# Performance work log

Measured on AMD Instinct MI355X. Metric: run time of the kernel, lower is better.

The kernel has to match this reference:

```python
import jax, jax.numpy as jnp
import numpy as np

B, N, D, H, A = 1024, 8, 256, 512, 4  # batch, num_objects, embedding_dim, hidden_dim, action_dim


def _edge_list(batch, n):
    # Fully connected (no self-loops) over n nodes, replicated per sample with offset b*n.
    pairs = np.array([(i, j) for i in range(n) for j in range(n) if i != j], dtype=np.int32)
    off = (np.arange(batch, dtype=np.int32) * n)[:, None]
    row = (pairs[:, 0][None, :] + off).reshape(-1)
    col = (pairs[:, 1][None, :] + off).reshape(-1)
    return jnp.asarray(row), jnp.asarray(col)


def _layer_norm(x, g, b):
    m = x.mean(-1, keepdims=True)
    v = x.var(-1, keepdims=True)
    return (x - m) / jnp.sqrt(v + 1e-5) * g + b


def _mlp(x, w1, b1, w2, b2, g, bn, w3, b3):
    h = jax.nn.relu(x @ w1 + b1)
    h = jax.nn.relu(_layer_norm(h @ w2 + b2, g, bn))
    return h @ w3 + b3


def setup_inputs() -> dict:
    key = jax.random.key(0)
    ks = jax.random.split(key, 12)
    def w(k, shape):
        return jax.random.normal(k, shape, jnp.float32) / np.sqrt(shape[0]).astype(np.float32)
    return {
        "states": jax.random.normal(ks[0], (B, N, D), jnp.float32),
        "action": jax.random.randint(ks[1], (B,), 0, A),
        # edge MLP: 3D -> H -> H (LN) -> H
        "e_w1": w(ks[2], (3 * D, H)), "e_b1": jnp.zeros((H,), jnp.float32),
        "e_w2": w(ks[3], (H, H)),     "e_b2": jnp.zeros((H,), jnp.float32),
        "e_g":  jnp.ones((H,), jnp.float32), "e_bn": jnp.zeros((H,), jnp.float32),
        "e_w3": w(ks[4], (H, H)),     "e_b3": jnp.zeros((H,), jnp.float32),
        # node MLP: H + D + A -> H -> H (LN) -> D
        "n_w1": w(ks[5], (H + D + A, H)), "n_b1": jnp.zeros((H,), jnp.float32),
        "n_w2": w(ks[6], (H, H)),         "n_b2": jnp.zeros((H,), jnp.float32),
        "n_g":  jnp.ones((H,), jnp.float32), "n_bn": jnp.zeros((H,), jnp.float32),
        "n_w3": w(ks[7], (H, D)),         "n_b3": jnp.zeros((D,), jnp.float32),
    }


def reference(states, action,
              e_w1, e_b1, e_w2, e_b2, e_g, e_bn, e_w3, e_b3,
              n_w1, n_b1, n_w2, n_b2, n_g, n_bn, n_w3, n_b3):
    eP = (e_w1, e_b1, e_w2, e_b2, e_g, e_bn, e_w3, e_b3)
    nP = (n_w1, n_b1, n_w2, n_b2, n_g, n_bn, n_w3, n_b3)
    flat = states.reshape(-1, D)                       # [B*N, D]
    row, col = _edge_list(B, N - 1)                    # faithful: edge list over N-1 objects
    E = row.shape[0]
    # copy_action / embodied: one-hot action repeated per object
    av = jnp.repeat(jax.nn.one_hot(action, A, dtype=flat.dtype), N, axis=0)  # [B*N, A]
    # round 0: edge_attr starts as zeros like node features
    e = _mlp(jnp.concatenate([flat[row], jnp.zeros((E, D), flat.dtype), flat[col]], 1), *eP)
    agg = jax.ops.segment_sum(e, row, num_segments=B * N)  # [B*N, H]
    node = _mlp(jnp.concatenate([flat, av, agg], 1), *nP)   # [B*N, D]
    flat = flat + node
    av0 = jnp.zeros_like(av)
    for _ in range(N - 1):
        e = _mlp(jnp.concatenate([flat[row], node[row], flat[col]], 1), *eP)
        agg = jax.ops.segment_sum(e, row, num_segments=B * N)
        node = _mlp(jnp.concatenate([flat, av0, agg], 1), *nP)
        flat = flat + node
    return flat.reshape(B, N, D)
```

## Files before the change

### kernel.cpp

```cpp
#include <hip/hip_runtime.h>
#include <cstddef>

typedef _Float16 f16x8 __attribute__((ext_vector_type(8)));
typedef _Float16 f16x4 __attribute__((ext_vector_type(4)));
typedef float f32x16 __attribute__((ext_vector_type(16)));
typedef unsigned short ushort_t;

#define NSEG 7168
#define NNODE 8192

enum { EP_NONE = 0, EP_BIAS = 1, EP_RAWP = 2, EP_NL1 = 3, EP_NL3 = 4 };

#define PHASE_BARRIER() do { asm volatile("s_waitcnt lgkmcnt(0)" ::: "memory"); \
                             __builtin_amdgcn_s_barrier(); } while (0)

#define RELU8(v) do { _Pragma("unroll") \
  for (int j_ = 0; j_ < 8; ++j_) v[j_] = v[j_] > (_Float16)0 ? v[j_] : (_Float16)0; } while (0)

__global__ __launch_bounds__(256)
void prepack(const float* __restrict__ W, ushort_t* __restrict__ P,
             int koff, int kcnt, int Nsrc, int NTpack, int noff) {
  int idx = blockIdx.x * 256 + threadIdx.x;
  if (idx >= kcnt * Nsrc) return;
  int kl = idx / Nsrc, n = idx - kl * Nsrc + noff;
  _Float16 h = (_Float16)W[idx];
  int k = koff + kl;
  size_t o = ((((size_t)(k >> 4)) * NTpack + (n >> 5)) * 64 + ((k >> 3) & 1) * 32 + (n & 31)) * 8 + (k & 7);
  P[o] = __builtin_bit_cast(ushort_t, h);
}

__global__ __launch_bounds__(256)
void v6k(const float* __restrict__ eb3, const float* __restrict__ nw1,
         float* __restrict__ v6) {
  int n = blockIdx.x * 256 + threadIdx.x;
  if (n >= 512) return;
  float a = 0.f;
  for (int k = 0; k < 512; ++k) a += eb3[k] * nw1[(size_t)(260 + k) * 512 + n];
  v6[n] = 6.f * a;
}

template <int NCOLB, int EPI, int EDGE, int LNIN, int X1F16, int OUTF16>
__global__ __launch_bounds__(256, 4)
void gemmT(const void* __restrict__ X1v, int ld1, int nph1,
           const void* __restrict__ X2v, int ld2, int nph2,
           const ushort_t* __restrict__ Sm, const ushort_t* __restrict__ Tm,
           const ushort_t* __restrict__ P,
           const float* __restrict__ bias, const float* __restrict__ bias2,
           const int* __restrict__ action, const float* __restrict__ wact,
           const float* __restrict__ lnpart,
           const float* __restrict__ lng, const float* __restrict__ lnbn,
           void* __restrict__ Yv, float* __restrict__ Yres,
           float* __restrict__ Part, int m0base) {
  constexpr int N = NCOLB * 128;
  constexpr int NT = N / 32;
  const int u = threadIdx.x;
  const int nwg = gridDim.x;
  const int qq = nwg >> 3, r8 = nwg & 7;
  const int xcd = blockIdx.x & 7, inx = blockIdx.x >> 3;
  const int logical = (xcd < r8 ? xcd * (qq + 1) : r8 * (qq + 1) + (xcd - r8) * qq) + inx;
  const int mY = (logical / NCOLB) * 64;
  const int cb = logical - (logical / NCOLB) * NCOLB;
  const int nB = cb * 128;
  const int lane = u & 63, w = u >> 6;
  const int wr = w >> 1, wc = w & 1;
  const int r31 = lane & 31, rt2 = lane >> 5;

  __shared__ ushort_t lA[16384];

  const int kcA = w * 2, kcB = w * 2 + 1;
  const int widx0 = (((rt2 * 8 + kcA) * 2 + 0) * 32 + (r31 ^ ((kcA & 3) << 3))) * 8;
  const int widx1 = (((rt2 * 8 + kcA) * 2 + 1) * 32 + (r31 ^ ((kcA & 3) << 3))) * 8;
  const int widx2 = (((rt2 * 8 + kcB) * 2 + 0) * 32 + (r31 ^ ((kcB & 3) << 3))) * 8;
  const int widx3 = (((rt2 * 8 + kcB) * 2 + 1) * 32 + (r31 ^ ((kcB & 3) << 3))) * 8;

  const ushort_t* sB = nullptr;
  const ushort_t* tB = nullptr;
  const float* x1f = nullptr;
  const ushort_t* x1h = nullptr;
  const ushort_t* x2h = nullptr;
  if (EDGE) {
    int e = m0base + mY + lane;
    int b = e / 42, p = e - b * 42;
    int i = p / 6, tt = p - i * 6;
    int j = tt + (tt >= i ? 1 : 0);
    sB = Sm + (size_t)(b * 7 + i) * 1024 + w * 32;
    tB = Tm + (size_t)(b * 7 + j) * 1024 + w * 32;
  } else {
    if (X1F16) x1h = (const ushort_t*)X1v + (size_t)(mY + lane) * ld1 + w * 32;
    else       x1f = (const float*)X1v + (size_t)(mY + lane) * ld1 + w * 32;
    if (nph2 > 0) x2h = (const ushort_t*)X2v + (size_t)(mY + lane) * ld2 + w * 32;
  }
  float mym = 0.f, myr = 0.f;
  if (LNIN) {
    const float* pp = lnpart + (size_t)(mY + lane) * 16;
    float S_ = 0.f, Q_ = 0.f;
    #pragma unroll
    for (int i = 0; i < 8; ++i) { S_ += pp[i]; Q_ += pp[8 + i]; }
    mym = S_ * (1.f / 512.f);
    myr = rsqrtf(Q_ * (1.f / 512.f) - mym * mym + 1e-5f);
  }

  f16x8 xc0, xc1, xc2, xc3;
  auto loadx = [&](int ph) {
    if (EDGE) {
      const ushort_t* sp = sB + ph * 128;
      const ushort_t* tp = tB + ph * 128;
      f16x8 s0 = *(const f16x8*)sp,        t0 = *(const f16x8*)tp;
      f16x8 s1 = *(const f16x8*)(sp + 8),  t1 = *(const f16x8*)(tp + 8);
      f16x8 s2 = *(const f16x8*)(sp + 16), t2 = *(const f16x8*)(tp + 16);
      f16x8 s3 = *(const f16x8*)(sp + 24), t3 = *(const f16x8*)(tp + 24);
      xc0 = s0 + t0; xc1 = s1 + t1; xc2 = s2 + t2; xc3 = s3 + t3;
      RELU8(xc0); RELU8(xc1); RELU8(xc2); RELU8(xc3);
    } else if (!X1F16 && ph < nph1) {
      const float* src = x1f + ph * 128;
      float4 l0 = *(const float4*)(src +  0), h0 = *(const float4*)(src +  4);
      float4 l1 = *(const float4*)(src +  8), h1 = *(const float4*)(src + 12);
      float4 l2 = *(const float4*)(src + 16), h2 = *(const float4*)(src + 20);
      float4 l3 = *(const float4*)(src + 24), h3 = *(const float4*)(src + 28);
#define CVT8(X, lo, hi) do { X[0]=(_Float16)lo.x; X[1]=(_Float16)lo.y; \
      X[2]=(_Float16)lo.z; X[3]=(_Float16)lo.w; X[4]=(_Float16)hi.x; \
      X[5]=(_Float16)hi.y; X[6]=(_Float16)hi.z; X[7]=(_Float16)hi.w; } while (0)
      CVT8(xc0, l0, h0); CVT8(xc1, l1, h1); CVT8(xc2, l2, h2); CVT8(xc3, l3, h3);
#undef CVT8
    } else {
      const ushort_t* src = (ph < nph1) ? x1h + ph * 128 : x2h + (ph - nph1) * 128;
      xc0 = *(const f16x8*)src;
      xc1 = *(const f16x8*)(src + 8);
      xc2 = *(const f16x8*)(src + 16);
      xc3 = *(const f16x8*)(src + 24);
      if (LNIN) {
        const int kb = ph * 128 + w * 32;
#define LN8(X, OFS) do { _Pragma("unroll") for (int j_ = 0; j_ < 8; ++j_) { \
        float xx = (float)X[j_]; \
        xx = fmaxf((xx - mym) * myr * lng[kb + (OFS) + j_] + lnbn[kb + (OFS) + j_], 0.f); \
        X[j_] = (_Float16)xx; } } while (0)
        LN8(xc0, 0); LN8(xc1, 8); LN8(xc2, 16); LN8(xc3, 24);
#undef LN8
      }
    }
  };
  auto cvtwrite = [&](int b) {
    const int base = b * 8192;
    *(f16x8*)&lA[base + widx0] = xc0;
    *(f16x8*)&lA[base + widx1] = xc1;
    *(f16x8*)&lA[base + widx2] = xc2;
    *(f16x8*)&lA[base + widx3] = xc3;
  };

  f32x16 acc0, acc1;
  #pragma unroll
  for (int q = 0; q < 16; ++q) { acc0[q] = 0.f; acc1[q] = 0.f; }

  const int nph = nph1 + nph2;
  const int ntb = (nB >> 5) + wc * 2;
  const int TOT = nph * 8;

#define LOADA(S, A_) do { \
    const int aofs_ = lbase + (((wr * 8 + (S)) * 2 + rt2) * 32 + (r31 ^ (((S) & 3) << 3))) * 8; \
    A_ = *(const f16x8*)&lA[aofs_]; } while (0)

#define LOADB(G_, H0, H1) do { \
    const ushort_t* bp_ = P + (((size_t)(G_) * NT + ntb) * 64 + lane) * 8; \
    H0 = *(const f16x8*)bp_; \
    H1 = *(const f16x8*)(bp_ + 512); } while (0)

#define MFMA2(AH, H0, H1) do { \
    acc0 = __builtin_amdgcn_mfma_f32_32x32x16_f16(AH, H0, acc0, 0, 0, 0); \
    acc1 = __builtin_amdgcn_mfma_f32_32x32x16_f16(AH, H1, acc1, 0, 0, 0); } while (0)

  loadx(0);
  cvtwrite(0);
  if (nph > 1) loadx(1);
  PHASE_BARRIER();
  f16x8 b00, b01, b10, b11, b20, b21, b30, b31;
  LOADB(0, b00, b01);
  LOADB(1, b10, b11);
  LOADB(2, b20, b21);
  LOADB(3, b30, b31);

  #pragma unroll 1
  for (int ph = 0; ph < nph; ++ph) {
    if (ph + 1 < nph) {
      cvtwrite((ph + 1) & 1);
      if (ph + 2 < nph) loadx(ph + 2);
    }
    const int lbase = (ph & 1) * 8192;
    const int g0 = ph * 8;
    f16x8 ac, an;
    LOADA(0, ac);
#define STEP(S, BH, BL) do { \
    if ((S) < 7) LOADA((S) + 1, an); \
    f16x8 h0 = BH, h1 = BL; \
    if (g0 + (S) + 4 < TOT) LOADB(g0 + (S) + 4, BH, BL); \
    MFMA2(ac, h0, h1); \
    if ((S) < 7) ac = an; } while (0)
    STEP(0, b00, b01);
    STEP(1, b10, b11);
    STEP(2, b20, b21);
    STEP(3, b30, b31);
    STEP(4, b00, b01);
    STEP(5, b10, b11);
    STEP(6, b20, b21);
    STEP(7, b30, b31);
#undef STEP
    if (ph + 1 < nph) PHASE_BARRIER();
  }

  const int col0 = nB + wc * 64 + r31;
  float v[2][16];
  {
    float bc0 = (EPI == EP_NONE) ? 0.f : bias[col0];
    float bc1 = (EPI == EP_NONE) ? 0.f : bias[col0 + 32];
    #pragma unroll
    for (int q = 0; q < 16; ++q) {
      v[0][q] = acc0[q] + bc0;
      v[1][q] = acc1[q] + bc1;
    }
  }

  if (EPI == EP_NL1) {
    #pragma unroll
    for (int q = 0; q < 16; ++q) {
      int m = mY + wr * 32 + (q & 3) + 8 * (q >> 2) + 4 * rt2;
      if (m < NSEG) {
        v[0][q] += bias2[col0];
        v[1][q] += bias2[col0 + 32];
      }
      if (action != nullptr) {
        const float* wrp = wact + (size_t)(256 + action[m >> 3]) * 512;
        v[0][q] += wrp[col0];
        v[1][q] += wrp[col0 + 32];
      }
    }
    #pragma unroll
    for (int ct = 0; ct < 2; ++ct)
      #pragma unroll
      for (int q = 0; q < 16; ++q) v[ct][q] = fmaxf(v[ct][q], 0.f);
  }

  if (EPI == EP_RAWP) {
    float sv[16], qv[16];
    #pragma unroll
    for (int q = 0; q < 16; ++q) {
      sv[q] = v[0][q] + v[1][q];
      qv[q] = v[0][q] * v[0][q] + v[1][q] * v[1][q];
    }
    #pragma unroll
    for (int mm = 1; mm <= 16; mm <<= 1) {
      #pragma unroll
      for (int q = 0; q < 16; ++q) {
        sv[q] += __shfl_xor(sv[q], mm);
        qv[q] += __shfl_xor(qv[q], mm);
      }
    }
    if (r31 == 0) {
      #pragma unroll
      for (int q = 0; q < 16; ++q) {
        int m = mY + wr * 32 + (q & 3) + 8 * (q >> 2) + 4 * rt2;
        Part[(size_t)m * 16 + cb * 2 + wc] = sv[q];
        Part[(size_t)m * 16 + 8 + cb * 2 + wc] = qv[q];
      }
    }
  }

  #pragma unroll
  for (int ct = 0; ct < 2; ++ct) {
    #pragma unroll
    for (int q = 0; q < 16; ++q) {
      int m = mY + wr * 32 + (q & 3) + 8 * (q >> 2) + 4 * rt2;
      float z = v[ct][q];
      if (OUTF16)
        ((ushort_t*)Yv)[(size_t)m * N + col0 + ct * 32] =
            __builtin_bit_cast(ushort_t, (_Float16)z);
      else
        ((float*)Yv)[(size_t)m * N + col0 + ct * 32] = z;
      if (EPI == EP_NL3) Yres[(size_t)m * N + col0 + ct * 32] += z;
    }
  }
#undef LOADA
#undef LOADB
#undef MFMA2
}

__global__ __launch_bounds__(256)
void h2_sum_ln(const ushort_t* __restrict__ H2, const float* __restrict__ Part,
               const float* __restrict__ g, const float* __restrict__ bn,
               ushort_t* __restrict__ SS) {
  __shared__ float smu[12], srs[12];
  const int u = threadIdx.x;
  const int g2 = blockIdx.x * 2;
  if (u < 12) {
    const float* pp = Part + ((size_t)g2 * 6 + u) * 16;
    float S = 0.f, Q = 0.f;
    #pragma unroll
    for (int i = 0; i < 8; ++i) { S += pp[i]; Q += pp[8 + i]; }
    float m = S * (1.f / 512.f);
    smu[u] = m;
    srs[u] = rsqrtf(Q * (1.f / 512.f) - m * m + 1e-5f);
  }
  __syncthreads();
  const int ln = g2 + (u >> 7);
  const int lloc = (u >> 7) * 6;
  const int c4 = (u & 127) * 4;
  float4 gv = *(const float4*)(g + c4);
  float4 bv = *(const float4*)(bn + c4);
  float a0 = 0.f, a1 = 0.f, a2 = 0.f, a3 = 0.f;
  #pragma unroll
  for (int r = 0; r < 6; ++r) {
    int row = ln * 6 + r;
    f16x4 y = *(const f16x4*)(H2 + (size_t)row * 512 + c4);
    float m = smu[lloc + r], rs = srs[lloc + r];
    a0 += fmaxf(((float)y[0] - m) * rs * gv.x + bv.x, 0.f);
    a1 += fmaxf(((float)y[1] - m) * rs * gv.y + bv.y, 0.f);
    a2 += fmaxf(((float)y[2] - m) * rs * gv.z + bv.z, 0.f);
    a3 += fmaxf(((float)y[3] - m) * rs * gv.w + bv.w, 0.f);
  }
  f16x4 o;
  o[0] = (_Float16)a0; o[1] = (_Float16)a1; o[2] = (_Float16)a2; o[3] = (_Float16)a3;
  *(f16x4*)(SS + (size_t)ln * 512 + c4) = o;
}

extern "C" void kernel_launch(void* const* d_in, const int* in_sizes, int n_in,
                              void* d_out, int out_size, void* d_ws, size_t ws_size,
                              hipStream_t stream) {
  (void)in_sizes; (void)n_in; (void)out_size;
  const float* states = (const float*)d_in[0];
  const int* action = (const int*)d_in[1];
  const float* e_w1 = (const float*)d_in[2];
  const float* e_b1 = (const float*)d_in[3];
  const float* e_w2 = (const float*)d_in[4];
  const float* e_b2 = (const float*)d_in[5];
  const float* e_g = (const float*)d_in[6];
  const float* e_bn = (const float*)d_in[7];
  const float* e_w3 = (const float*)d_in[8];
  const float* e_b3 = (const float*)d_in[9];
  const float* n_w1 = (const float*)d_in[10];
  const float* n_b1 = (const float*)d_in[11];
  const float* n_w2 = (const float*)d_in[12];
  const float* n_b2 = (const float*)d_in[13];
  const float* n_g = (const float*)d_in[14];
  const float* n_bn = (const float*)d_in[15];
  const float* n_w3 = (const float*)d_in[16];
  const float* n_b3 = (const float*)d_in[17];

  float* flat = (float*)d_out;
  float* fp = (float*)d_ws;
  float* Mbuf = fp;  fp += 262144;
  float* v6 = fp;    fp += 512;
  float* b1ext = fp; fp += 1024;
  float* PartE = fp; fp += 688128;
  float* PartN = fp; fp += 131072;
  ushort_t* us = (ushort_t*)fp;
  ushort_t* node = us; us += 2097152;
  ushort_t* SS = us;   us += 4194304;
  ushort_t* G = us;    us += 4194304;
  ushort_t* G2 = us;   us += 4194304;
  ushort_t* STb = us;  us += 7340032;
  ushort_t* PeST = us; us += 524288;
  ushort_t* PeW2 = us; us += 262144;
  ushort_t* Ptmp = us; us += 262144;
  ushort_t* PnW1M = us; us += 393216;
  ushort_t* PnW2 = us;  us += 262144;
  ushort_t* PnW3 = us;  us += 131072;
  ushort_t* H2 = us;

  const size_t fixedB = (size_t)((char*)H2 - (char*)d_ws);
  int nc = 32;
  for (int cand = 1; cand <= 32; cand <<= 1)
    if (fixedB + (43008ull / cand) * 512ull * 2ull <= ws_size) { nc = cand; break; }
  const int spc = 1024 / nc;
  const int epc = spc * 42;

  hipMemsetAsync(PeST, 0, 524288 * 2, stream);
  prepack<<<1024, 256, 0, stream>>>(e_w1, PeST, 0, 512, 512, 32, 0);
  prepack<<<512, 256, 0, stream>>>(e_w1 + 262144, PeST, 0, 256, 512, 32, 512);
  prepack<<<1024, 256, 0, stream>>>(e_w2, PeW2, 0, 512, 512, 16, 0);
  prepack<<<1024, 256, 0, stream>>>(n_w1 + 133120, Ptmp, 0, 512, 512, 16, 0);
  prepack<<<512, 256, 0, stream>>>(n_w1, PnW1M, 0, 256, 512, 16, 0);
  prepack<<<1024, 256, 0, stream>>>(n_w2, PnW2, 0, 512, 512, 16, 0);
  prepack<<<512, 256, 0, stream>>>(n_w3, PnW3, 0, 512, 256, 8, 0);
  hipMemcpyAsync(b1ext, e_b1, 512 * 4, hipMemcpyDeviceToDevice, stream);
  hipMemsetAsync(b1ext + 512, 0, 512 * 4, stream);
  gemmT<4, EP_NONE, 0, 0, 0, 0><<<32, 256, 0, stream>>>(
      e_w3, 512, 4, nullptr, 0, 0, nullptr, nullptr, Ptmp, nullptr, nullptr,
      nullptr, nullptr, nullptr, nullptr, nullptr, Mbuf, nullptr, nullptr, 0);
  prepack<<<1024, 256, 0, stream>>>(Mbuf, PnW1M, 256, 512, 512, 16, 0);
  v6k<<<2, 256, 0, stream>>>(e_b3, n_w1, v6);
  hipMemsetAsync(SS + (size_t)NSEG * 512, 0, (size_t)(NNODE - NSEG) * 512 * 2, stream);
  hipMemcpyAsync(flat, states, (size_t)NNODE * 256 * 4, hipMemcpyDeviceToDevice, stream);

  for (int round = 0; round < 8; ++round) {
    if (round == 0)
      gemmT<8, EP_BIAS, 0, 0, 0, 1><<<896, 256, 0, stream>>>(
          flat, 256, 2, nullptr, 0, 0, nullptr, nullptr, PeST, b1ext, nullptr,
          nullptr, nullptr, nullptr, nullptr, nullptr, STb, nullptr, nullptr, 0);
    else
      gemmT<8, EP_BIAS, 0, 0, 0, 1><<<896, 256, 0, stream>>>(
          flat, 256, 2, node, 256, 2, nullptr, nullptr, PeST, b1ext, nullptr,
          nullptr, nullptr, nullptr, nullptr, nullptr, STb, nullptr, nullptr, 0);
    for (int ch = 0; ch < nc; ++ch) {
      gemmT<4, EP_RAWP, 1, 0, 0, 1><<<(epc / 64) * 4, 256, 0, stream>>>(
          nullptr, 0, 4, nullptr, 0, 0, STb, STb + 512, PeW2, e_b2, nullptr,
          nullptr, nullptr, nullptr, nullptr, nullptr,
          H2, nullptr, PartE, ch * epc);
      h2_sum_ln<<<(spc * 7) / 2, 256, 0, stream>>>(
          H2, PartE, e_g, e_bn, SS + (size_t)ch * spc * 7 * 512);
    }
    gemmT<4, EP_NL1, 0, 0, 0, 1><<<512, 256, 0, stream>>>(
        flat, 256, 2, SS, 512, 4, nullptr, nullptr, PnW1M, n_b1, v6,
        (round == 0) ? action : nullptr, n_w1,
        nullptr, nullptr, nullptr, G, nullptr, nullptr, 0);
    gemmT<4, EP_RAWP, 0, 0, 1, 1><<<512, 256, 0, stream>>>(
        G, 512, 4, nullptr, 0, 0, nullptr, nullptr, PnW2, n_b2, nullptr,
        nullptr, nullptr, nullptr, nullptr, nullptr, G2, nullptr, PartN, 0);
    gemmT<2, EP_NL3, 0, 1, 1, 1><<<256, 256, 0, stream>>>(
        G2, 512, 4, nullptr, 0, 0, nullptr, nullptr, PnW3, n_b3, nullptr,
        nullptr, nullptr, PartN, n_g, n_bn, node, flat, nullptr, 0);
  }
}
```

Measured before the change: 1.282 ms.

## Stage whole A tile in LDS once and stream B with register prefetch

Adds a gemmS kernel that loads the entire 64-row A tile (all K chunks) into shared memory in one pass with a single barrier. The K loop then runs without per-phase barriers, and B fragments are prefetched four chunks ahead into registers. Most GEMMs, including the edge MLP second layer, switch to it, while gemmT is kept only for the weight-fusion GEMM and the node first layer. The larger LDS footprint (up to 64 KB) and lower launch-bound occupancy (2 instead of 4) trade parallelism for fewer synchronisations.

```diff
diff --git a/kernel.cpp b/kernel.cpp
--- a/kernel.cpp
+++ b/kernel.cpp
@@ -39,10 +39,10 @@
   v6[n] = 6.f * a;
 }
 
-template <int NCOLB, int EPI, int EDGE, int LNIN, int X1F16, int OUTF16>
-__global__ __launch_bounds__(256, 4)
-void gemmT(const void* __restrict__ X1v, int ld1, int nph1,
-           const void* __restrict__ X2v, int ld2, int nph2,
+template <int NCOLB, int TOTC, int EPI, int EDGE, int LNIN, int X1F16, int OUTF16>
+__global__ __launch_bounds__(256, 2)
+void gemmS(const void* __restrict__ X1v, int ld1, int nch1,
+           const void* __restrict__ X2v, int ld2,
            const ushort_t* __restrict__ Sm, const ushort_t* __restrict__ Tm,
            const ushort_t* __restrict__ P,
            const float* __restrict__ bias, const float* __restrict__ bias2,
@@ -51,6 +51,230 @@
            const float* __restrict__ lng, const float* __restrict__ lnbn,
            void* __restrict__ Yv, float* __restrict__ Yres,
            float* __restrict__ Part, int m0base) {
+  constexpr int N = NCOLB * 128;
+  constexpr int NT = N / 32;
+  constexpr int CPT = TOTC / 4;
+  const int u = threadIdx.x;
+  const int nwg = gridDim.x;
+  const int qq = nwg >> 3, r8 = nwg & 7;
+  const int xcd = blockIdx.x & 7, inx = blockIdx.x >> 3;
+  const int logical = (xcd < r8 ? xcd * (qq + 1) : r8 * (qq + 1) + (xcd - r8) * qq) + inx;
+  const int mY = (logical / NCOLB) * 64;
+  const int cb = logical - (logical / NCOLB) * NCOLB;
+  const int nB = cb * 128;
+  const int lane = u & 63, w = u >> 6;
+  const int wr = w >> 1, wc = w & 1;
+  const int r31 = lane & 31, rt2 = lane >> 5;
+
+  __shared__ ushort_t lA[TOTC * 1024];
+
+  const ushort_t* sA = nullptr;
+  const ushort_t* tA = nullptr;
+  const float* x1f = nullptr;
+  const ushort_t* x1h = nullptr;
+  const ushort_t* x2h = nullptr;
+  if (EDGE) {
+    int e = m0base + mY + lane;
+    int b = e / 42, p = e - b * 42;
+    int i = p / 6, tt = p - i * 6;
+    int j = tt + (tt >= i ? 1 : 0);
+    sA = Sm + (size_t)(b * 7 + i) * 1024;
+    tA = Tm + (size_t)(b * 7 + j) * 1024;
+  } else {
+    if (X1F16) x1h = (const ushort_t*)X1v + (size_t)(mY + lane) * ld1;
+    else       x1f = (const float*)X1v + (size_t)(mY + lane) * ld1;
+    if (X2v != nullptr) x2h = (const ushort_t*)X2v + (size_t)(mY + lane) * ld2;
+  }
+  float mym = 0.f, myr = 0.f;
+  if (LNIN) {
+    const float* pp = lnpart + (size_t)(mY + lane) * 16;
+    float S_ = 0.f, Q_ = 0.f;
+    #pragma unroll
+    for (int i = 0; i < 8; ++i) { S_ += pp[i]; Q_ += pp[8 + i]; }
+    mym = S_ * (1.f / 512.f);
+    myr = rsqrtf(Q_ * (1.f / 512.f) - mym * mym + 1e-5f);
+  }
+
+  {
+    f16x8 xs0[CPT], xs1[CPT];
+    #pragma unroll
+    for (int j = 0; j < CPT; ++j) {
+      const int c = w * CPT + j;
+      if (EDGE) {
+        const ushort_t* sp = sA + c * 16;
+        const ushort_t* tp = tA + c * 16;
+        f16x8 s0 = *(const f16x8*)sp, t0 = *(const f16x8*)tp;
+        f16x8 s1 = *(const f16x8*)(sp + 8), t1 = *(const f16x8*)(tp + 8);
+        xs0[j] = s0 + t0; xs1[j] = s1 + t1;
+        RELU8(xs0[j]); RELU8(xs1[j]);
+      } else if (!X1F16 && c < nch1) {
+        const float* src = x1f + c * 16;
+        float4 a0 = *(const float4*)(src + 0),  a1 = *(const float4*)(src + 4);
+        float4 a2 = *(const float4*)(src + 8),  a3 = *(const float4*)(src + 12);
+        xs0[j][0] = (_Float16)a0.x; xs0[j][1] = (_Float16)a0.y;
+        xs0[j][2] = (_Float16)a0.z; xs0[j][3] = (_Float16)a0.w;
+        xs0[j][4] = (_Float16)a1.x; xs0[j][5] = (_Float16)a1.y;
+        xs0[j][6] = (_Float16)a1.z; xs0[j][7] = (_Float16)a1.w;
+        xs1[j][0] = (_Float16)a2.x; xs1[j][1] = (_Float16)a2.y;
+        xs1[j][2] = (_Float16)a2.z; xs1[j][3] = (_Float16)a2.w;
+        xs1[j][4] = (_Float16)a3.x; xs1[j][5] = (_Float16)a3.y;
+        xs1[j][6] = (_Float16)a3.z; xs1[j][7] = (_Float16)a3.w;
+      } else {
+        const ushort_t* src = (c < nch1) ? x1h + c * 16 : x2h + (c - nch1) * 16;
+        xs0[j] = *(const f16x8*)src;
+        xs1[j] = *(const f16x8*)(src + 8);
+        if (LNIN) {
+          const int kb = c * 16;
+          #pragma unroll
+          for (int j_ = 0; j_ < 8; ++j_) {
+            float xx = (float)xs0[j][j_];
+            xx = fmaxf((xx - mym) * myr * lng[kb + j_] + lnbn[kb + j_], 0.f);
+            xs0[j][j_] = (_Float16)xx;
+            float yy = (float)xs1[j][j_];
+            yy = fmaxf((yy - mym) * myr * lng[kb + 8 + j_] + lnbn[kb + 8 + j_], 0.f);
+            xs1[j][j_] = (_Float16)yy;
+          }
+        }
+      }
+    }
+    #pragma unroll
+    for (int j = 0; j < CPT; ++j) {
+      const int c = w * CPT + j;
+      const int o0 = (((rt2 * TOTC + c) * 2 + 0) * 32 + (r31 ^ ((c & 3) << 3))) * 8;
+      *(f16x8*)&lA[o0] = xs0[j];
+      *(f16x8*)&lA[o0 + 256] = xs1[j];
+    }
+  }
+
+  f32x16 acc0, acc1;
+  #pragma unroll
+  for (int q = 0; q < 16; ++q) { acc0[q] = 0.f; acc1[q] = 0.f; }
+  const int ntb = (nB >> 5) + wc * 2;
+
+#define LOADA(C, A_) do { \
+    const int aofs_ = (((wr * TOTC + (C)) * 2 + rt2) * 32 + (r31 ^ (((C) & 3) << 3))) * 8; \
+    A_ = *(const f16x8*)&lA[aofs_]; } while (0)
+
+#define LOADB(G_, H0, H1) do { \
+    const ushort_t* bp_ = P + (((size_t)(G_) * NT + ntb) * 64 + lane) * 8; \
+    H0 = *(const f16x8*)bp_; \
+    H1 = *(const f16x8*)(bp_ + 512); } while (0)
+
+#define MFMA2(AH, H0, H1) do { \
+    acc0 = __builtin_amdgcn_mfma_f32_32x32x16_f16(AH, H0, acc0, 0, 0, 0); \
+    acc1 = __builtin_amdgcn_mfma_f32_32x32x16_f16(AH, H1, acc1, 0, 0, 0); } while (0)
+
+  f16x8 b00, b01, b10, b11, b20, b21, b30, b31;
+  LOADB(0, b00, b01);
+  LOADB(1, b10, b11);
+  LOADB(2, b20, b21);
+  LOADB(3, b30, b31);
+  PHASE_BARRIER();
+
+  f16x8 ac, an;
+  LOADA(0, ac);
+#define STEPS(C, BH, BL) do { \
+    if ((C) + 1 < TOTC) LOADA((C) + 1, an); \
+    f16x8 h0 = BH, h1 = BL; \
+    if ((C) + 4 < TOTC) LOADB((C) + 4, BH, BL); \
+    MFMA2(ac, h0, h1); \
+    if ((C) + 1 < TOTC) ac = an; } while (0)
+  #pragma unroll
+  for (int c4 = 0; c4 < TOTC; c4 += 4) {
+    STEPS(c4 + 0, b00, b01);
+    STEPS(c4 + 1, b10, b11);
+    STEPS(c4 + 2, b20, b21);
+    STEPS(c4 + 3, b30, b31);
+  }
+#undef STEPS
+
+  const int col0 = nB + wc * 64 + r31;
+  float v[2][16];
+  {
+    float bc0 = (EPI == EP_NONE) ? 0.f : bias[col0];
+    float bc1 = (EPI == EP_NONE) ? 0.f : bias[col0 + 32];
+    #pragma unroll
+    for (int q = 0; q < 16; ++q) {
+      v[0][q] = acc0[q] + bc0;
+      v[1][q] = acc1[q] + bc1;
+    }
+  }
+
+  if (EPI == EP_NL1) {
+    #pragma unroll
+    for (int q = 0; q < 16; ++q) {
+      int m = mY + wr * 32 + (q & 3) + 8 * (q >> 2) + 4 * rt2;
+      if (m < NSEG) {
+        v[0][q] += bias2[col0];
+        v[1][q] += bias2[col0 + 32];
+      }
+      if (action != nullptr) {
+        const float* wrp = wact + (size_t)(256 + action[m >> 3]) * 512;
+        v[0][q] += wrp[col0];
+        v[1][q] += wrp[col0 + 32];
+      }
+    }
+    #pragma unroll
+    for (int ct = 0; ct < 2; ++ct)
+      #pragma unroll
+      for (int q = 0; q < 16; ++q) v[ct][q] = fmaxf(v[ct][q], 0.f);
+  }
+
+  if (EPI == EP_RAWP) {
+    float sv[16], qv[16];
+    #pragma unroll
+    for (int q = 0; q < 16; ++q) {
+      sv[q] = v[0][q] + v[1][q];
+      qv[q] = v[0][q] * v[0][q] + v[1][q] * v[1][q];
+    }
+    #pragma unroll
+    for (int mm = 1; mm <= 16; mm <<= 1) {
+      #pragma unroll
+      for (int q = 0; q < 16; ++q) {
+        sv[q] += __shfl_xor(sv[q], mm);
+        qv[q] += __shfl_xor(qv[q], mm);
+      }
+    }
+    if (r31 == 0) {
+      #pragma unroll
+      for (int q = 0; q < 16; ++q) {
+        int m = mY + wr * 32 + (q & 3) + 8 * (q >> 2) + 4 * rt2;
+        Part[(size_t)m * 16 + cb * 2 + wc] = sv[q];
+        Part[(size_t)m * 16 + 8 + cb * 2 + wc] = qv[q];
+      }
+    }
+  }
+
+  #pragma unroll
+  for (int ct = 0; ct < 2; ++ct) {
+    #pragma unroll
+    for (int q = 0; q < 16; ++q) {
+      int m = mY + wr * 32 + (q & 3) + 8 * (q >> 2) + 4 * rt2;
+      float z = v[ct][q];
+      if (OUTF16)
+        ((ushort_t*)Yv)[(size_t)m * N + col0 + ct * 32] =
+            __builtin_bit_cast(ushort_t, (_Float16)z);
+      else
+        ((float*)Yv)[(size_t)m * N + col0 + ct * 32] = z;
+      if (EPI == EP_NL3) Yres[(size_t)m * N + col0 + ct * 32] += z;
+    }
+  }
+#undef LOADA
+#undef LOADB
+#undef MFMA2
+}
+
+template <int NCOLB, int EPI, int LNIN, int X1F16, int OUTF16>
+__global__ __launch_bounds__(256, 4)
+void gemmT(const void* __restrict__ X1v, int ld1, int nph1,
+           const void* __restrict__ X2v, int ld2, int nph2,
+           const ushort_t* __restrict__ P,
+           const float* __restrict__ bias, const float* __restrict__ bias2,
+           const int* __restrict__ action, const float* __restrict__ wact,
+           const float* __restrict__ lnpart,
+           const float* __restrict__ lng, const float* __restrict__ lnbn,
+           void* __restrict__ Yv, float* __restrict__ Yres,
+           float* __restrict__ Part) {
   constexpr int N = NCOLB * 128;
   constexpr int NT = N / 32;
   const int u = threadIdx.x;
@@ -73,23 +297,13 @@
   const int widx2 = (((rt2 * 8 + kcB) * 2 + 0) * 32 + (r31 ^ ((kcB & 3) << 3))) * 8;
   const int widx3 = (((rt2 * 8 + kcB) * 2 + 1) * 32 + (r31 ^ ((kcB & 3) << 3))) * 8;
 
-  const ushort_t* sB = nullptr;
-  const ushort_t* tB = nullptr;
   const float* x1f = nullptr;
   const ushort_t* x1h = nullptr;
   const ushort_t* x2h = nullptr;
-  if (EDGE) {
-    int e = m0base + mY + lane;
-    int b = e / 42, p = e - b * 42;
-    int i = p / 6, tt = p - i * 6;
-    int j = tt + (tt >= i ? 1 : 0);
-    sB = Sm + (size_t)(b * 7 + i) * 1024 + w * 32;
-    tB = Tm + (size_t)(b * 7 + j) * 1024 + w * 32;
-  } else {
-    if (X1F16) x1h = (const ushort_t*)X1v + (size_t)(mY + lane) * ld1 + w * 32;
-    else       x1f = (const float*)X1v + (size_t)(mY + lane) * ld1 + w * 32;
-    if (nph2 > 0) x2h = (const ushort_t*)X2v + (size_t)(mY + lane) * ld2 + w * 32;
-  }
+  if (X1F16) x1h = (const ushort_t*)X1v + (size_t)(mY + lane) * ld1 + w * 32;
+  else       x1f = (const float*)X1v + (size_t)(mY + lane) * ld1 + w * 32;
+  if (nph2 > 0) x2h = (const ushort_t*)X2v + (size_t)(mY + lane) * ld2 + w * 32;
+
   float mym = 0.f, myr = 0.f;
   if (LNIN) {
     const float* pp = lnpart + (size_t)(mY + lane) * 16;
@@ -102,16 +316,7 @@
 
   f16x8 xc0, xc1, xc2, xc3;
   auto loadx = [&](int ph) {
-    if (EDGE) {
-      const ushort_t* sp = sB + ph * 128;
-      const ushort_t* tp = tB + ph * 128;
-      f16x8 s0 = *(const f16x8*)sp,        t0 = *(const f16x8*)tp;
-      f16x8 s1 = *(const f16x8*)(sp + 8),  t1 = *(const f16x8*)(tp + 8);
-      f16x8 s2 = *(const f16x8*)(sp + 16), t2 = *(const f16x8*)(tp + 16);
-      f16x8 s3 = *(const f16x8*)(sp + 24), t3 = *(const f16x8*)(tp + 24);
-      xc0 = s0 + t0; xc1 = s1 + t1; xc2 = s2 + t2; xc3 = s3 + t3;
-      RELU8(xc0); RELU8(xc1); RELU8(xc2); RELU8(xc3);
-    } else if (!X1F16 && ph < nph1) {
+    if (!X1F16 && ph < nph1) {
       const float* src = x1f + ph * 128;
       float4 l0 = *(const float4*)(src +  0), h0 = *(const float4*)(src +  4);
       float4 l1 = *(const float4*)(src +  8), h1 = *(const float4*)(src + 12);
@@ -128,15 +333,6 @@
       xc1 = *(const f16x8*)(src + 8);
       xc2 = *(const f16x8*)(src + 16);
       xc3 = *(const f16x8*)(src + 24);
-      if (LNIN) {
-        const int kb = ph * 128 + w * 32;
-#define LN8(X, OFS) do { _Pragma("unroll") for (int j_ = 0; j_ < 8; ++j_) { \
-        float xx = (float)X[j_]; \
-        xx = fmaxf((xx - mym) * myr * lng[kb + (OFS) + j_] + lnbn[kb + (OFS) + j_], 0.f); \
-        X[j_] = (_Float16)xx; } } while (0)
-        LN8(xc0, 0); LN8(xc1, 8); LN8(xc2, 16); LN8(xc3, 24);
-#undef LN8
-      }
     }
   };
   auto cvtwrite = [&](int b) {
@@ -381,9 +577,9 @@
   prepack<<<512, 256, 0, stream>>>(n_w3, PnW3, 0, 512, 256, 8, 0);
   hipMemcpyAsync(b1ext, e_b1, 512 * 4, hipMemcpyDeviceToDevice, stream);
   hipMemsetAsync(b1ext + 512, 0, 512 * 4, stream);
-  gemmT<4, EP_NONE, 0, 0, 0, 0><<<32, 256, 0, stream>>>(
-      e_w3, 512, 4, nullptr, 0, 0, nullptr, nullptr, Ptmp, nullptr, nullptr,
-      nullptr, nullptr, nullptr, nullptr, nullptr, Mbuf, nullptr, nullptr, 0);
+  gemmT<4, EP_NONE, 0, 0, 0><<<32, 256, 0, stream>>>(
+      e_w3, 512, 4, nullptr, 0, 0, Ptmp, nullptr, nullptr,
+      nullptr, nullptr, nullptr, nullptr, nullptr, Mbuf, nullptr, nullptr);
   prepack<<<1024, 256, 0, stream>>>(Mbuf, PnW1M, 256, 512, 512, 16, 0);
   v6k<<<2, 256, 0, stream>>>(e_b3, n_w1, v6);
   hipMemsetAsync(SS + (size_t)NSEG * 512, 0, (size_t)(NNODE - NSEG) * 512 * 2, stream);
@@ -391,30 +587,30 @@
 
   for (int round = 0; round < 8; ++round) {
     if (round == 0)
-      gemmT<8, EP_BIAS, 0, 0, 0, 1><<<896, 256, 0, stream>>>(
-          flat, 256, 2, nullptr, 0, 0, nullptr, nullptr, PeST, b1ext, nullptr,
+      gemmS<8, 16, EP_BIAS, 0, 0, 0, 1><<<896, 256, 0, stream>>>(
+          flat, 256, 16, nullptr, 0, nullptr, nullptr, PeST, b1ext, nullptr,
           nullptr, nullptr, nullptr, nullptr, nullptr, STb, nullptr, nullptr, 0);
     else
-      gemmT<8, EP_BIAS, 0, 0, 0, 1><<<896, 256, 0, stream>>>(
-          flat, 256, 2, node, 256, 2, nullptr, nullptr, PeST, b1ext, nullptr,
+      gemmS<8, 32, EP_BIAS, 0, 0, 0, 1><<<896, 256, 0, stream>>>(
+          flat, 256, 16, node, 256, nullptr, nullptr, PeST, b1ext, nullptr,
           nullptr, nullptr, nullptr, nullptr, nullptr, STb, nullptr, nullptr, 0);
     for (int ch = 0; ch < nc; ++ch) {
-      gemmT<4, EP_RAWP, 1, 0, 0, 1><<<(epc / 64) * 4, 256, 0, stream>>>(
-          nullptr, 0, 4, nullptr, 0, 0, STb, STb + 512, PeW2, e_b2, nullptr,
+      gemmS<4, 32, EP_RAWP, 1, 0, 0, 1><<<(epc / 64) * 4, 256, 0, stream>>>(
+          nullptr, 0, 32, nullptr, 0, STb, STb + 512, PeW2, e_b2, nullptr,
           nullptr, nullptr, nullptr, nullptr, nullptr,
           H2, nullptr, PartE, ch * epc);
       h2_sum_ln<<<(spc * 7) / 2, 256, 0, stream>>>(
           H2, PartE, e_g, e_bn, SS + (size_t)ch * spc * 7 * 512);
     }
-    gemmT<4, EP_NL1, 0, 0, 0, 1><<<512, 256, 0, stream>>>(
-        flat, 256, 2, SS, 512, 4, nullptr, nullptr, PnW1M, n_b1, v6,
+    gemmT<4, EP_NL1, 0, 0, 1><<<512, 256, 0, stream>>>(
+        flat, 256, 2, SS, 512, 4, PnW1M, n_b1, v6,
         (round == 0) ? action : nullptr, n_w1,
-        nullptr, nullptr, nullptr, G, nullptr, nullptr, 0);
-    gemmT<4, EP_RAWP, 0, 0, 1, 1><<<512, 256, 0, stream>>>(
-        G, 512, 4, nullptr, 0, 0, nullptr, nullptr, PnW2, n_b2, nullptr,
+        nullptr, nullptr, nullptr, G, nullptr, nullptr);
+    gemmS<4, 32, EP_RAWP, 0, 0, 1, 1><<<512, 256, 0, stream>>>(
+        G, 512, 32, nullptr, 0, nullptr, nullptr, PnW2, n_b2, nullptr,
         nullptr, nullptr, nullptr, nullptr, nullptr, G2, nullptr, PartN, 0);
-    gemmT<2, EP_NL3, 0, 1, 1, 1><<<256, 256, 0, stream>>>(
-        G2, 512, 4, nullptr, 0, 0, nullptr, nullptr, PnW3, n_b3, nullptr,
+    gemmS<2, 32, EP_NL3, 0, 1, 1, 1><<<256, 256, 0, stream>>>(
+        G2, 512, 32, nullptr, 0, nullptr, nullptr, PnW3, n_b3, nullptr,
         nullptr, nullptr, PartN, n_g, n_bn, node, flat, nullptr, 0);
   }
 }
```

Result: slower. 1.438 ms (+12.2%).

## Fuse edge GEMM, LayerNorm and segment sum into one full-width kernel

Applied to the files above, without the earlier changes.

Replaces the chunked edge-layer pipeline (gemmT edge GEMM writing H2 plus partial stats, then h2_sum_ln) with one 1024-thread edge_fused kernel. Each block computes the full 512-column H2 tile for 64 edges, does the LayerNorm row statistics in-block, applies ReLU and accumulates per-segment sums in LDS. Results go to an fp32 aggregate buffer, using atomics only for segments shared across block boundaries. This removes the H2 round trip through global memory and the many per-chunk launches. In exchange it adds a per-round memset of the fp32 aggregate and a node GEMM that reads fp32 input, and runs a large-LDS block that may limit occupancy.

```diff
diff --git a/kernel.cpp b/kernel.cpp
--- a/kernel.cpp
+++ b/kernel.cpp
@@ -2,7 +2,6 @@
 #include <cstddef>
 
 typedef _Float16 f16x8 __attribute__((ext_vector_type(8)));
-typedef _Float16 f16x4 __attribute__((ext_vector_type(4)));
 typedef float f32x16 __attribute__((ext_vector_type(16)));
 typedef unsigned short ushort_t;
 
@@ -39,18 +38,17 @@
   v6[n] = 6.f * a;
 }
 
-template <int NCOLB, int EPI, int EDGE, int LNIN, int X1F16, int OUTF16>
+template <int NCOLB, int EPI, int LNIN, int X1F16, int X2F32, int OUTF16>
 __global__ __launch_bounds__(256, 4)
 void gemmT(const void* __restrict__ X1v, int ld1, int nph1,
            const void* __restrict__ X2v, int ld2, int nph2,
-           const ushort_t* __restrict__ Sm, const ushort_t* __restrict__ Tm,
            const ushort_t* __restrict__ P,
            const float* __restrict__ bias, const float* __restrict__ bias2,
            const int* __restrict__ action, const float* __restrict__ wact,
            const float* __restrict__ lnpart,
            const float* __restrict__ lng, const float* __restrict__ lnbn,
            void* __restrict__ Yv, float* __restrict__ Yres,
-           float* __restrict__ Part, int m0base) {
+           float* __restrict__ Part) {
   constexpr int N = NCOLB * 128;
   constexpr int NT = N / 32;
   const int u = threadIdx.x;
@@ -73,23 +71,17 @@
   const int widx2 = (((rt2 * 8 + kcB) * 2 + 0) * 32 + (r31 ^ ((kcB & 3) << 3))) * 8;
   const int widx3 = (((rt2 * 8 + kcB) * 2 + 1) * 32 + (r31 ^ ((kcB & 3) << 3))) * 8;
 
-  const ushort_t* sB = nullptr;
-  const ushort_t* tB = nullptr;
   const float* x1f = nullptr;
   const ushort_t* x1h = nullptr;
+  const float* x2f = nullptr;
   const ushort_t* x2h = nullptr;
-  if (EDGE) {
-    int e = m0base + mY + lane;
-    int b = e / 42, p = e - b * 42;
-    int i = p / 6, tt = p - i * 6;
-    int j = tt + (tt >= i ? 1 : 0);
-    sB = Sm + (size_t)(b * 7 + i) * 1024 + w * 32;
-    tB = Tm + (size_t)(b * 7 + j) * 1024 + w * 32;
-  } else {
-    if (X1F16) x1h = (const ushort_t*)X1v + (size_t)(mY + lane) * ld1 + w * 32;
-    else       x1f = (const float*)X1v + (size_t)(mY + lane) * ld1 + w * 32;
-    if (nph2 > 0) x2h = (const ushort_t*)X2v + (size_t)(mY + lane) * ld2 + w * 32;
-  }
+  if (X1F16) x1h = (const ushort_t*)X1v + (size_t)(mY + lane) * ld1 + w * 32;
+  else       x1f = (const float*)X1v + (size_t)(mY + lane) * ld1 + w * 32;
+  if (nph2 > 0) {
+    if (X2F32) x2f = (const float*)X2v + (size_t)(mY + lane) * ld2 + w * 32;
+    else       x2h = (const ushort_t*)X2v + (size_t)(mY + lane) * ld2 + w * 32;
+  }
+
   float mym = 0.f, myr = 0.f;
   if (LNIN) {
     const float* pp = lnpart + (size_t)(mY + lane) * 16;
@@ -101,34 +93,28 @@
   }
 
   f16x8 xc0, xc1, xc2, xc3;
+#define CVT8(X, lo, hi) do { X[0]=(_Float16)lo.x; X[1]=(_Float16)lo.y; \
+    X[2]=(_Float16)lo.z; X[3]=(_Float16)lo.w; X[4]=(_Float16)hi.x; \
+    X[5]=(_Float16)hi.y; X[6]=(_Float16)hi.z; X[7]=(_Float16)hi.w; } while (0)
+  auto loadf32 = [&](const float* src) {
+    float4 l0 = *(const float4*)(src +  0), h0 = *(const float4*)(src +  4);
+    float4 l1 = *(const float4*)(src +  8), h1 = *(const float4*)(src + 12);
+    float4 l2 = *(const float4*)(src + 16), h2 = *(const float4*)(src + 20);
+    float4 l3 = *(const float4*)(src + 24), h3 = *(const float4*)(src + 28);
+    CVT8(xc0, l0, h0); CVT8(xc1, l1, h1); CVT8(xc2, l2, h2); CVT8(xc3, l3, h3);
+  };
   auto loadx = [&](int ph) {
-    if (EDGE) {
-      const ushort_t* sp = sB + ph * 128;
-      const ushort_t* tp = tB + ph * 128;
-      f16x8 s0 = *(const f16x8*)sp,        t0 = *(const f16x8*)tp;
-      f16x8 s1 = *(const f16x8*)(sp + 8),  t1 = *(const f16x8*)(tp + 8);
-      f16x8 s2 = *(const f16x8*)(sp + 16), t2 = *(const f16x8*)(tp + 16);
-      f16x8 s3 = *(const f16x8*)(sp + 24), t3 = *(const f16x8*)(tp + 24);
-      xc0 = s0 + t0; xc1 = s1 + t1; xc2 = s2 + t2; xc3 = s3 + t3;
-      RELU8(xc0); RELU8(xc1); RELU8(xc2); RELU8(xc3);
-    } else if (!X1F16 && ph < nph1) {
-      const float* src = x1f + ph * 128;
-      float4 l0 = *(const float4*)(src +  0), h0 = *(const float4*)(src +  4);
-      float4 l1 = *(const float4*)(src +  8), h1 = *(const float4*)(src + 12);
-      float4 l2 = *(const float4*)(src + 16), h2 = *(const float4*)(src + 20);
-      float4 l3 = *(const float4*)(src + 24), h3 = *(const float4*)(src + 28);
-#define CVT8(X, lo, hi) do { X[0]=(_Float16)lo.x; X[1]=(_Float16)lo.y; \
-      X[2]=(_Float16)lo.z; X[3]=(_Float16)lo.w; X[4]=(_Float16)hi.x; \
-      X[5]=(_Float16)hi.y; X[6]=(_Float16)hi.z; X[7]=(_Float16)hi.w; } while (0)
-      CVT8(xc0, l0, h0); CVT8(xc1, l1, h1); CVT8(xc2, l2, h2); CVT8(xc3, l3, h3);
-#undef CVT8
+    if (!X1F16 && ph < nph1) {
+      loadf32(x1f + ph * 128);
+    } else if (X2F32 && ph >= nph1) {
+      loadf32(x2f + (ph - nph1) * 128);
     } else {
       const ushort_t* src = (ph < nph1) ? x1h + ph * 128 : x2h + (ph - nph1) * 128;
       xc0 = *(const f16x8*)src;
       xc1 = *(const f16x8*)(src + 8);
       xc2 = *(const f16x8*)(src + 16);
       xc3 = *(const f16x8*)(src + 24);
-      if (LNIN) {
+      if (LNIN && X1F16) {
         const int kb = ph * 128 + w * 32;
 #define LN8(X, OFS) do { _Pragma("unroll") for (int j_ = 0; j_ < 8; ++j_) { \
         float xx = (float)X[j_]; \
@@ -139,6 +125,7 @@
       }
     }
   };
+#undef CVT8
   auto cvtwrite = [&](int b) {
     const int base = b * 8192;
     *(f16x8*)&lA[base + widx0] = xc0;
@@ -282,48 +269,189 @@
 #undef MFMA2
 }
 
-__global__ __launch_bounds__(256)
-void h2_sum_ln(const ushort_t* __restrict__ H2, const float* __restrict__ Part,
-               const float* __restrict__ g, const float* __restrict__ bn,
-               ushort_t* __restrict__ SS) {
-  __shared__ float smu[12], srs[12];
+__global__ __launch_bounds__(1024, 4)
+void edge_fused(const ushort_t* __restrict__ Sm, const ushort_t* __restrict__ Tm,
+                const ushort_t* __restrict__ P,
+                const float* __restrict__ bias,
+                const float* __restrict__ g, const float* __restrict__ bn,
+                float* __restrict__ SS) {
   const int u = threadIdx.x;
-  const int g2 = blockIdx.x * 2;
-  if (u < 12) {
-    const float* pp = Part + ((size_t)g2 * 6 + u) * 16;
-    float S = 0.f, Q = 0.f;
-    #pragma unroll
-    for (int i = 0; i < 8; ++i) { S += pp[i]; Q += pp[8 + i]; }
-    float m = S * (1.f / 512.f);
-    smu[u] = m;
-    srs[u] = rsqrtf(Q * (1.f / 512.f) - m * m + 1e-5f);
+  const int nwg = gridDim.x;
+  const int xcd = blockIdx.x & 7, inx = blockIdx.x >> 3;
+  const int blk = xcd * (nwg >> 3) + inx;
+  const int e0 = blk * 64;
+  const int lane = u & 63, w = u >> 6;
+  const int r31 = lane & 31, rt2 = lane >> 5;
+  const int wrh = w >> 3, wcq = w & 7;
+
+  __shared__ ushort_t lA[16384];
+  __shared__ float SSloc[12][512];
+  __shared__ float sS[64][8], sQ[64][8];
+  __shared__ float muL[64], rsL[64];
+
+  #pragma unroll
+  for (int i = 0; i < 6; ++i) ((float*)SSloc)[u + 1024 * i] = 0.f;
+
+  {
+  }
+  int e = e0 + lane;
+  int b = e / 42, p = e - b * 42;
+  int ii = p / 6, tt = p - ii * 6;
+  int jj = tt + (tt >= ii ? 1 : 0);
+  const ushort_t* sA = Sm + (size_t)(b * 7 + ii) * 1024;
+  const ushort_t* tA = Tm + (size_t)(b * 7 + jj) * 1024;
+  const int kc = w >> 1, khi = w & 1;
+  const int koff = kc * 16 + khi * 8;
+  const int widx = (((rt2 * 8 + kc) * 2 + khi) * 32 + (r31 ^ ((kc & 3) << 3))) * 8;
+
+  f16x8 xc;
+  auto loadx = [&](int ph) {
+    f16x8 s = *(const f16x8*)(sA + ph * 128 + koff);
+    f16x8 t = *(const f16x8*)(tA + ph * 128 + koff);
+    xc = s + t;
+    RELU8(xc);
+  };
+  auto cvtwrite = [&](int bb) { *(f16x8*)&lA[bb * 8192 + widx] = xc; };
+
+  f32x16 acc0, acc1;
+  #pragma unroll
+  for (int q = 0; q < 16; ++q) { acc0[q] = 0.f; acc1[q] = 0.f; }
+
+#define LOADA(S, A_) do { \
+    const int aofs_ = lbase + (((wrh * 8 + (S)) * 2 + rt2) * 32 + (r31 ^ (((S) & 3) << 3))) * 8; \
+    A_ = *(const f16x8*)&lA[aofs_]; } while (0)
+
+#define LOADB(G_, H0, H1) do { \
+    const ushort_t* bp_ = P + (((size_t)(G_) * 16 + wcq * 2) * 64 + lane) * 8; \
+    H0 = *(const f16x8*)bp_; \
+    H1 = *(const f16x8*)(bp_ + 512); } while (0)
+
+#define MFMA2(AH, H0, H1) do { \
+    acc0 = __builtin_amdgcn_mfma_f32_32x32x16_f16(AH, H0, acc0, 0, 0, 0); \
+    acc1 = __builtin_amdgcn_mfma_f32_32x32x16_f16(AH, H1, acc1, 0, 0, 0); } while (0)
+
+  loadx(0);
+  cvtwrite(0);
+  loadx(1);
+  PHASE_BARRIER();
+  f16x8 b00, b01, b10, b11, b20, b21, b30, b31;
+  LOADB(0, b00, b01);
+  LOADB(1, b10, b11);
+  LOADB(2, b20, b21);
+  LOADB(3, b30, b31);
+
+  #pragma unroll 1
+  for (int ph = 0; ph < 4; ++ph) {
+    if (ph + 1 < 4) {
+      cvtwrite((ph + 1) & 1);
+      if (ph + 2 < 4) loadx(ph + 2);
+    }
+    const int lbase = (ph & 1) * 8192;
+    const int g0 = ph * 8;
+    f16x8 ac, an;
+    LOADA(0, ac);
+#define STEP(S, BH, BL) do { \
+    if ((S) < 7) LOADA((S) + 1, an); \
+    f16x8 h0 = BH, h1 = BL; \
+    if (g0 + (S) + 4 < 32) LOADB(g0 + (S) + 4, BH, BL); \
+    MFMA2(ac, h0, h1); \
+    if ((S) < 7) ac = an; } while (0)
+    STEP(0, b00, b01);
+    STEP(1, b10, b11);
+    STEP(2, b20, b21);
+    STEP(3, b30, b31);
+    STEP(4, b00, b01);
+    STEP(5, b10, b11);
+    STEP(6, b20, b21);
+    STEP(7, b30, b31);
+#undef STEP
+    if (ph + 1 < 4) PHASE_BARRIER();
+  }
+#undef LOADA
+#undef LOADB
+#undef MFMA2
+
+  const int col0 = wcq * 64 + r31;
+  float v[2][16];
+  {
+    float bc0 = bias[col0], bc1 = bias[col0 + 32];
+    #pragma unroll
+    for (int q = 0; q < 16; ++q) {
+      v[0][q] = acc0[q] + bc0;
+      v[1][q] = acc1[q] + bc1;
+    }
+  }
+  {
+    float sv[16], qv[16];
+    #pragma unroll
+    for (int q = 0; q < 16; ++q) {
+      sv[q] = v[0][q] + v[1][q];
+      qv[q] = v[0][q] * v[0][q] + v[1][q] * v[1][q];
+    }
+    #pragma unroll
+    for (int mm = 1; mm <= 16; mm <<= 1) {
+      #pragma unroll
+      for (int q = 0; q < 16; ++q) {
+        sv[q] += __shfl_xor(sv[q], mm);
+        qv[q] += __shfl_xor(qv[q], mm);
+      }
+    }
+    if (r31 == 0) {
+      #pragma unroll
+      for (int q = 0; q < 16; ++q) {
+        int row = wrh * 32 + (q & 3) + 8 * (q >> 2) + 4 * rt2;
+        sS[row][wcq] = sv[q];
+        sQ[row][wcq] = qv[q];
+      }
+    }
   }
   __syncthreads();
-  const int ln = g2 + (u >> 7);
-  const int lloc = (u >> 7) * 6;
-  const int c4 = (u & 127) * 4;
-  float4 gv = *(const float4*)(g + c4);
-  float4 bv = *(const float4*)(bn + c4);
-  float a0 = 0.f, a1 = 0.f, a2 = 0.f, a3 = 0.f;
-  #pragma unroll
-  for (int r = 0; r < 6; ++r) {
-    int row = ln * 6 + r;
-    f16x4 y = *(const f16x4*)(H2 + (size_t)row * 512 + c4);
-    float m = smu[lloc + r], rs = srs[lloc + r];
-    a0 += fmaxf(((float)y[0] - m) * rs * gv.x + bv.x, 0.f);
-    a1 += fmaxf(((float)y[1] - m) * rs * gv.y + bv.y, 0.f);
-    a2 += fmaxf(((float)y[2] - m) * rs * gv.z + bv.z, 0.f);
-    a3 += fmaxf(((float)y[3] - m) * rs * gv.w + bv.w, 0.f);
-  }
-  f16x4 o;
-  o[0] = (_Float16)a0; o[1] = (_Float16)a1; o[2] = (_Float16)a2; o[3] = (_Float16)a3;
-  *(f16x4*)(SS + (size_t)ln * 512 + c4) = o;
+  if (u < 64) {
+    float S_ = 0.f, Q_ = 0.f;
+    #pragma unroll
+    for (int k = 0; k < 8; ++k) { S_ += sS[u][k]; Q_ += sQ[u][k]; }
+    float m = S_ * (1.f / 512.f);
+    muL[u] = m;
+    rsL[u] = rsqrtf(Q_ * (1.f / 512.f) - m * m + 1e-5f);
+  }
+  __syncthreads();
+  const int segbase = (int)(__umulhi((unsigned)e0, 0xAAAAAAABu) >> 2);
+  {
+    float gc0 = g[col0], gc1 = g[col0 + 32];
+    float bn0 = bn[col0], bn1 = bn[col0 + 32];
+    #pragma unroll
+    for (int q = 0; q < 16; ++q) {
+      int row = wrh * 32 + (q & 3) + 8 * (q >> 2) + 4 * rt2;
+      float m = muL[row], rs = rsL[row];
+      int eg = e0 + row;
+      int si = (int)(__umulhi((unsigned)eg, 0xAAAAAAABu) >> 2) - segbase;
+      float z0 = fmaxf((v[0][q] - m) * rs * gc0 + bn0, 0.f);
+      float z1 = fmaxf((v[1][q] - m) * rs * gc1 + bn1, 0.f);
+      atomicAdd(&SSloc[si][col0], z0);
+      atomicAdd(&SSloc[si][col0 + 32], z1);
+    }
+  }
+  __syncthreads();
+  if (u < 512) {
+    const int seglast = (int)(__umulhi((unsigned)(e0 + 63), 0xAAAAAAABu) >> 2);
+    const int nseg = seglast - segbase + 1;
+    const bool loSh = (e0 - segbase * 6) != 0;
+    const bool hiSh = ((e0 + 64) - (seglast + ((e0 + 64 - seglast * 6 >= 6) ? 1 : 0)) * 6,
+                       ((e0 + 64) % 6) != 0) && (e0 + 64 < 43008);
+    for (int si = 0; si < nseg; ++si) {
+      int sg = segbase + si;
+      float val = SSloc[si][u];
+      bool at = (si == 0 && loSh) || (si == nseg - 1 && hiSh);
+      if (at) atomicAdd(&SS[(size_t)sg * 512 + u], val);
+      else SS[(size_t)sg * 512 + u] = val;
+    }
+  }
 }
 
 extern "C" void kernel_launch(void* const* d_in, const int* in_sizes, int n_in,
                               void* d_out, int out_size, void* d_ws, size_t ws_size,
                               hipStream_t stream) {
-  (void)in_sizes; (void)n_in; (void)out_size;
+  (void)in_sizes; (void)n_in; (void)out_size; (void)ws_size;
   const float* states = (const float*)d_in[0];
   const int* action = (const int*)d_in[1];
   const float* e_w1 = (const float*)d_in[2];
@@ -348,11 +476,10 @@
   float* Mbuf = fp;  fp += 262144;
   float* v6 = fp;    fp += 512;
   float* b1ext = fp; fp += 1024;
-  float* PartE = fp; fp += 688128;
   float* PartN = fp; fp += 131072;
+  float* SSf = fp;   fp += 4194304;
   ushort_t* us = (ushort_t*)fp;
   ushort_t* node = us; us += 2097152;
-  ushort_t* SS = us;   us += 4194304;
   ushort_t* G = us;    us += 4194304;
   ushort_t* G2 = us;   us += 4194304;
   ushort_t* STb = us;  us += 7340032;
@@ -362,14 +489,6 @@
   ushort_t* PnW1M = us; us += 393216;
   ushort_t* PnW2 = us;  us += 262144;
   ushort_t* PnW3 = us;  us += 131072;
-  ushort_t* H2 = us;
-
-  const size_t fixedB = (size_t)((char*)H2 - (char*)d_ws);
-  int nc = 32;
-  for (int cand = 1; cand <= 32; cand <<= 1)
-    if (fixedB + (43008ull / cand) * 512ull * 2ull <= ws_size) { nc = cand; break; }
-  const int spc = 1024 / nc;
-  const int epc = spc * 42;
 
   hipMemsetAsync(PeST, 0, 524288 * 2, stream);
   prepack<<<1024, 256, 0, stream>>>(e_w1, PeST, 0, 512, 512, 32, 0);
@@ -382,39 +501,32 @@
   hipMemcpyAsync(b1ext, e_b1, 512 * 4, hipMemcpyDeviceToDevice, stream);
   hipMemsetAsync(b1ext + 512, 0, 512 * 4, stream);
   gemmT<4, EP_NONE, 0, 0, 0, 0><<<32, 256, 0, stream>>>(
-      e_w3, 512, 4, nullptr, 0, 0, nullptr, nullptr, Ptmp, nullptr, nullptr,
-      nullptr, nullptr, nullptr, nullptr, nullptr, Mbuf, nullptr, nullptr, 0);
+      e_w3, 512, 4, nullptr, 0, 0, Ptmp, nullptr, nullptr,
+      nullptr, nullptr, nullptr, nullptr, nullptr, Mbuf, nullptr, nullptr);
   prepack<<<1024, 256, 0, stream>>>(Mbuf, PnW1M, 256, 512, 512, 16, 0);
   v6k<<<2, 256, 0, stream>>>(e_b3, n_w1, v6);
-  hipMemsetAsync(SS + (size_t)NSEG * 512, 0, (size_t)(NNODE - NSEG) * 512 * 2, stream);
   hipMemcpyAsync(flat, states, (size_t)NNODE * 256 * 4, hipMemcpyDeviceToDevice, stream);
 
   for (int round = 0; round < 8; ++round) {
     if (round == 0)
       gemmT<8, EP_BIAS, 0, 0, 0, 1><<<896, 256, 0, stream>>>(
-          flat, 256, 2, nullptr, 0, 0, nullptr, nullptr, PeST, b1ext, nullptr,
-          nullptr, nullptr, nullptr, nullptr, nullptr, STb, nullptr, nullptr, 0);
+          flat, 256, 2, nullptr, 0, 0, PeST, b1ext, nullptr,
+          nullptr, nullptr, nullptr, nullptr, nullptr, STb, nullptr, nullptr);
     else
       gemmT<8, EP_BIAS, 0, 0, 0, 1><<<896, 256, 0, stream>>>(
-          flat, 256, 2, node, 256, 2, nullptr, nullptr, PeST, b1ext, nullptr,
-          nullptr, nullptr, nullptr, nullptr, nullptr, STb, nullptr, nullptr, 0);
-    for (int ch = 0; ch < nc; ++ch) {
-      gemmT<4, EP_RAWP, 1, 0, 0, 1><<<(epc / 64) * 4, 256, 0, stream>>>(
-          nullptr, 0, 4, nullptr, 0, 0, STb, STb + 512, PeW2, e_b2, nullptr,
-          nullptr, nullptr, nullptr, nullptr, nullptr,
-          H2, nullptr, PartE, ch * epc);
-      h2_sum_ln<<<(spc * 7) / 2, 256, 0, stream>>>(
-          H2, PartE, e_g, e_bn, SS + (size_t)ch * spc * 7 * 512);
-    }
-    gemmT<4, EP_NL1, 0, 0, 0, 1><<<512, 256, 0, stream>>>(
-        flat, 256, 2, SS, 512, 4, nullptr, nullptr, PnW1M, n_b1, v6,
+          flat, 256, 2, node, 256, 2, PeST, b1ext, nullptr,
+          nullptr, nullptr, nullptr, nullptr, nullptr, STb, nullptr, nullptr);
+    hipMemsetAsync(SSf, 0, (size_t)NNODE * 512 * 4, stream);
+    edge_fused<<<672, 1024, 0, stream>>>(STb, STb + 512, PeW2, e_b2, e_g, e_bn, SSf);
+    gemmT<4, EP_NL1, 0, 0, 1, 1><<<512, 256, 0, stream>>>(
+        flat, 256, 2, SSf, 512, 4, PnW1M, n_b1, v6,
         (round == 0) ? action : nullptr, n_w1,
-        nullptr, nullptr, nullptr, G, nullptr, nullptr, 0);
-    gemmT<4, EP_RAWP, 0, 0, 1, 1><<<512, 256, 0, stream>>>(
-        G, 512, 4, nullptr, 0, 0, nullptr, nullptr, PnW2, n_b2, nullptr,
-        nullptr, nullptr, nullptr, nullptr, nullptr, G2, nullptr, PartN, 0);
-    gemmT<2, EP_NL3, 0, 1, 1, 1><<<256, 256, 0, stream>>>(
-        G2, 512, 4, nullptr, 0, 0, nullptr, nullptr, PnW3, n_b3, nullptr,
-        nullptr, nullptr, PartN, n_g, n_bn, node, flat, nullptr, 0);
+        nullptr, nullptr, nullptr, G, nullptr, nullptr);
+    gemmT<4, EP_RAWP, 0, 1, 0, 1><<<512, 256, 0, stream>>>(
+        G, 512, 4, nullptr, 0, 0, PnW2, n_b2, nullptr,
+        nullptr, nullptr, nullptr, nullptr, nullptr, G2, nullptr, PartN);
+    gemmT<2, EP_NL3, 1, 1, 0, 1><<<256, 256, 0, stream>>>(
+        G2, 512, 4, nullptr, 0, 0, PnW3, n_b3, nullptr,
+        nullptr, nullptr, PartN, n_g, n_bn, node, flat, nullptr);
   }
 }
```

New measurement: 2.273 ms. +77.3%, slower.
